# Kernel optimization log

Measured on AMD Instinct MI355X. Metric: run time of the kernel, lower is better.

Reference implementation:

```python
import jax, jax.numpy as jnp
import numpy as np
import math

D = 256
H = 128
GATE_IN = 2 * D + 1 + 1 + 3  # mu, logvar, s, minutes, snr(3) = 517


def setup_inputs() -> dict:
    key = jax.random.key(0)
    ks = jax.random.split(key, 10)
    B, S = 256, 512
    mu = jax.random.normal(ks[0], (B, S, D), dtype=jnp.float32)
    logvar = jax.random.normal(ks[1], (B, S, D), dtype=jnp.float32)
    minutes = jax.random.uniform(ks[2], (B, S), dtype=jnp.float32) * 120.0
    mu_c = jax.random.normal(ks[3], (2, D), dtype=jnp.float32) * 0.1
    log_tau2 = jax.random.normal(ks[4], (2, D), dtype=jnp.float32) * 0.1
    log_prior = jax.random.normal(ks[5], (2,), dtype=jnp.float32) * 0.1
    W1 = jax.random.normal(ks[6], (H, GATE_IN), dtype=jnp.float32) * 0.05
    b1 = jnp.zeros((H,), dtype=jnp.float32)
    W2 = jax.random.normal(ks[7], (1, H), dtype=jnp.float32) * 0.05
    b2 = jnp.zeros((1,), dtype=jnp.float32)
    alpha_logits = jnp.float32(0.0)          # logit(0.5)
    attn_lambda_logit = jnp.float32(0.0)     # logit(0.5)
    decay_rate_log = jnp.float32(math.log(0.1))
    return dict(mu=mu, logvar=logvar, minutes=minutes, mu_c=mu_c,
                log_tau2=log_tau2, log_prior=log_prior, W1=W1, b1=b1,
                W2=W2, b2=b2, alpha_logits=alpha_logits,
                attn_lambda_logit=attn_lambda_logit,
                decay_rate_log=decay_rate_log)


def _logit(p):
    return jnp.log(p) - jnp.log1p(-p)


def reference(mu, logvar, minutes, mu_c, log_tau2, log_prior,
              W1, b1, W2, b2, alpha_logits, attn_lambda_logit,
              decay_rate_log):
    var = jnp.exp(logvar)                              # [B,S,D]

    def ell(c):
        tau2 = jnp.exp(log_tau2[c])                    # [D]
        diff2 = (mu - mu_c[c]) ** 2
        return -0.5 * jnp.sum((var + diff2) / tau2 + log_tau2[c], axis=-1)

    s = (ell(1) + log_prior[1]) - (ell(0) + log_prior[0])   # [B,S]

    # SNR features
    var_c = jnp.clip(var, 1e-6, None)
    snr1 = jnp.linalg.norm(mu, axis=-1) / math.sqrt(mu.shape[-1])
    snr2 = jnp.mean(logvar, axis=-1)
    snr3 = jnp.mean(mu ** 2 / var_c, axis=-1)
    snr = jnp.stack([snr1, snr2, snr3], axis=-1)            # [B,S,3]

    gate_in = jnp.concatenate(
        [mu, logvar, s[..., None], minutes[..., None], snr], axis=-1)

    h = jax.nn.relu(jnp.einsum('bsf,hf->bsh', gate_in, W1) + b1)
    a_raw = jax.nn.sigmoid(jnp.einsum('bsh,oh->bso', h, W2) + b2)[..., 0]

    # precision attention mixture
    score = jnp.sum(mu ** 2 / var_c, axis=-1)               # [B,S]
    a_prec = jax.nn.softmax(score, axis=1)
    a_mlp = a_raw / jnp.clip(jnp.sum(a_raw, axis=1, keepdims=True), 1e-6, None)
    lam = jax.nn.sigmoid(attn_lambda_logit)
    a = lam * a_mlp + (1.0 - lam) * a_prec

    # time decay
    last_time = jnp.max(minutes, axis=1, keepdims=True)
    delta_h = jnp.clip(last_time - minutes, 0.0, None) / 60.0
    rate = jax.nn.softplus(decay_rate_log)
    w = a * jnp.exp(-rate * delta_h)
    a = w / jnp.clip(jnp.sum(w, axis=1, keepdims=True), 1e-6, None)

    # mean aggregator
    s_main = jnp.sum(a * s, axis=1)                         # [B]

    # Noisy-OR branch
    p_i = jnp.clip(jax.nn.sigmoid(s) * a, 1e-6, 1.0 - 1e-6)
    log1m = jnp.sum(jnp.log1p(-p_i), axis=1)
    p_or = 1.0 - jnp.exp(log1m)
    s_or = _logit(jnp.clip(p_or, 1e-6, 1.0 - 1e-6))

    alpha = jax.nn.sigmoid(alpha_logits)
    s_total = alpha * s_main + (1.0 - alpha) * s_or
    return (s_total, s, a)
```

## Files before the change

### kernel.cpp

```cpp
#include <hip/hip_runtime.h>
#include <hip/hip_bf16.h>

#define B_DIM 256
#define NTOK (256 * 512)
#define W1_LD 517
#define TPB 32

#define WS_DIT 0
#define WS_E 256
#define WS_C0 512
#define WS_W1F 1024
#define WS_W1X 17408
#define WS_SCORE 20480

typedef __attribute__((ext_vector_type(8))) short bf16x8;
typedef __attribute__((ext_vector_type(4))) float f32x4;
typedef long long i64;

__device__ __forceinline__ unsigned pk2(float a, float b) {
  __hip_bfloat162 h = __float22bfloat162_rn(make_float2(a, b));
  unsigned r;
  __builtin_memcpy(&r, &h, 4);
  return r;
}
__device__ __forceinline__ unsigned pk4f8(float a, float b, float c, float d) {
  int r = __builtin_amdgcn_cvt_pk_fp8_f32(a, b, 0, false);
  r = __builtin_amdgcn_cvt_pk_fp8_f32(c, d, r, true);
  return (unsigned)r;
}

template <int CTRL>
__device__ __forceinline__ float dpp_add(float v) {
  int s = __builtin_amdgcn_update_dpp(0, __float_as_int(v), CTRL, 0xf, 0xf,
                                      true);
  return v + __int_as_float(s);
}
__device__ __forceinline__ float row8_sum(float v) {
  v = dpp_add<0xB1>(v);
  v = dpp_add<0x4E>(v);
  v = dpp_add<0x141>(v);
  return v;
}
__device__ __forceinline__ float row16_sum(float v) {
  v = dpp_add<0xB1>(v);
  v = dpp_add<0x4E>(v);
  v = dpp_add<0x124>(v);
  v = dpp_add<0x128>(v);
  return v;
}

__device__ __forceinline__ float wave_sum(float v) {
#pragma unroll
  for (int off = 32; off > 0; off >>= 1) v += __shfl_xor(v, off, 64);
  return v;
}
__device__ __forceinline__ float wave_max(float v) {
#pragma unroll
  for (int off = 32; off > 0; off >>= 1) v = fmaxf(v, __shfl_xor(v, off, 64));
  return v;
}
__device__ __forceinline__ float block_sum(float v, float* scr) {
  v = wave_sum(v);
  int wid = threadIdx.x >> 6;
  __syncthreads();
  if ((threadIdx.x & 63) == 0) scr[wid] = v;
  __syncthreads();
  return scr[0] + scr[1] + scr[2] + scr[3];
}

__global__ __launch_bounds__(256) void k_setup(
    const float* __restrict__ W1, const float* __restrict__ b1,
    const float* __restrict__ mu_c, const float* __restrict__ log_tau2,
    const float* __restrict__ log_prior, float* __restrict__ wsc) {
  const int tid = threadIdx.x;
  const int h = blockIdx.x;
  const float* wr = W1 + h * W1_LD;
  {
    const int p = 2 * tid;
    const int c0 = ((p & 15) < 8) ? (p >> 4) * 8 + (p & 7)
                                  : 256 + (p >> 4) * 8 + (p & 7);
    const int p1 = p + 1;
    const int c1 = ((p1 & 15) < 8) ? (p1 >> 4) * 8 + (p1 & 7)
                                   : 256 + (p1 >> 4) * 8 + (p1 & 7);
    const int pk = __builtin_amdgcn_cvt_pk_fp8_f32(wr[c0], wr[c1], 0, false);
    char* w1f = (char*)(wsc + WS_W1F);
    const int off = (h >> 4) * 8192 + (p >> 5) * 512 +
                    (((p >> 3) & 3) * 16 + (h & 15)) * 8 + (p & 7);
    *(ushort*)(w1f + off) = (ushort)pk;
  }
  if (tid == 0) {
    ushort* w1x = (ushort*)(wsc + WS_W1X);
    const int nb = (h >> 4) * 512;
    uint4 g0;
    g0.x = pk2(wr[512], wr[513]);
    g0.y = pk2(wr[514], wr[515]);
    g0.z = pk2(wr[516], b1[h]);
    g0.w = 0u;
    *(uint4*)(w1x + nb + (h & 15) * 8) = g0;
    const uint4 z = {0u, 0u, 0u, 0u};
    *(uint4*)(w1x + nb + (16 + (h & 15)) * 8) = z;
    *(uint4*)(w1x + nb + (32 + (h & 15)) * 8) = z;
    *(uint4*)(w1x + nb + (48 + (h & 15)) * 8) = z;
  }

  if (blockIdx.x == 0) {
    __shared__ float scr[4];
    float lt0 = log_tau2[tid], lt1 = log_tau2[256 + tid];
    float mc0 = mu_c[tid], mc1 = mu_c[256 + tid];
    float it0 = __expf(-lt0), it1 = __expf(-lt1);
    wsc[WS_DIT + tid] = it1 - it0;
    wsc[WS_E + tid] = 2.0f * (mc1 * it1 - mc0 * it0);
    float g = mc1 * mc1 * it1 - mc0 * mc0 * it0 + (lt1 - lt0);
    float sg = block_sum(g, scr);
    if (tid == 0) wsc[WS_C0] = (log_prior[1] - log_prior[0]) - 0.5f * sg;
  }
}

__global__ __launch_bounds__(256, 8) void k_token(
    const float* __restrict__ mu, const float* __restrict__ logvar,
    const float* __restrict__ minutes, const float* __restrict__ W2g,
    const float* __restrict__ b2, const float* __restrict__ wsc,
    float* __restrict__ out_s, float* __restrict__ ws_score,
    float* __restrict__ araw_out) {
  __shared__ __align__(16) char A_l[TPB * 512];
  __shared__ __align__(16) ushort axl[TPB * 32];
  __shared__ float red2[4][TPB];

  const int tid = threadIdx.x;
  const int w = tid >> 6;
  const int l = tid & 63;
  const int tokbase = blockIdx.x * TPB;
  const float C0 = wsc[WS_C0];

  if (tid < 96) {
    const int row = tid & 31;
    const int c = tid >> 5;
    const uint4 z = {0u, 0u, 0u, 0u};
    *(uint4*)((char*)axl + row * 64 + 16 + c * 16) = z;
  }

  const int trow = tid >> 3;
  const int l8 = tid & 7;
  const int swz = (trow & 7) << 4;
  const size_t gbase = (size_t)(tokbase + trow) * 256 + l8 * 8;
  const float* ditg = wsc + WS_DIT + l8 * 8;
  const float* eg = wsc + WS_E + l8 * 8;
  float Ss = 0.f, Sm = 0.f, Sl = 0.f, Sc = 0.f;
#pragma unroll
  for (int t = 0; t < 4; ++t) {
    const float4 m0 = *(const float4*)(mu + gbase + t * 64);
    const float4 m1 = *(const float4*)(mu + gbase + t * 64 + 4);
    const float4 v0 = *(const float4*)(logvar + gbase + t * 64);
    const float4 v1 = *(const float4*)(logvar + gbase + t * 64 + 4);
    const float4 dA = *(const float4*)(ditg + t * 64);
    const float4 dB = *(const float4*)(ditg + t * 64 + 4);
    const float4 eA = *(const float4*)(eg + t * 64);
    const float4 eB = *(const float4*)(eg + t * 64 + 4);
#define CHUNK(m, lv, dt, ee)                                              \
  {                                                                       \
    const float va = __expf(lv.x), vb = __expf(lv.y), vc = __expf(lv.z),  \
                vd = __expf(lv.w);                                        \
    const float na = __expf(-lv.x), nb = __expf(-lv.y),                   \
                nc = __expf(-lv.z), nd = __expf(-lv.w);                   \
    const float qa = m.x * m.x, qb = m.y * m.y, qc = m.z * m.z,           \
                qd = m.w * m.w;                                           \
    Ss += (va + qa) * dt.x - m.x * ee.x + (vb + qb) * dt.y - m.y * ee.y + \
          (vc + qc) * dt.z - m.z * ee.z + (vd + qd) * dt.w - m.w * ee.w;  \
    Sm += qa + qb + qc + qd;                                              \
    Sl += lv.x + lv.y + lv.z + lv.w;                                      \
    Sc += qa * na + qb * nb + qc * nc + qd * nd;                          \
  }
    CHUNK(m0, v0, dA, eA);
    CHUNK(m1, v1, dB, eB);
#undef CHUNK
    uint4 u;
    u.x = pk4f8(m0.x, m0.y, m0.z, m0.w);
    u.y = pk4f8(m1.x, m1.y, m1.z, m1.w);
    u.z = pk4f8(v0.x, v0.y, v0.z, v0.w);
    u.w = pk4f8(v1.x, v1.y, v1.z, v1.w);
    const int col = trow * 512 + (t * 8 + l8) * 16;
    *(uint4*)(A_l + (col ^ swz)) = u;
  }
  Ss = row8_sum(Ss);
  Sm = row8_sum(Sm);
  Sl = row8_sum(Sl);
  Sc = row8_sum(Sc);
  if (l8 == 0) {
    const float sval = -0.5f * Ss + C0;
    const float mn = minutes[tokbase + trow];
    uint4 ex;
    ex.x = pk2(sval, mn);
    ex.y = pk2(sqrtf(Sm) * (1.0f / 16.0f), Sl * (1.0f / 256.0f));
    ex.z = pk2(Sc * (1.0f / 256.0f), 1.0f);
    ex.w = 0u;
    *(uint4*)((char*)axl + trow * 64) = ex;
    out_s[tokbase + trow] = sval;
    ws_score[tokbase + trow] = Sc;
  }
  __syncthreads();

  f32x4 a00 = {0.f, 0.f, 0.f, 0.f};
  f32x4 a01 = {0.f, 0.f, 0.f, 0.f};
  f32x4 a10 = {0.f, 0.f, 0.f, 0.f};
  f32x4 a11 = {0.f, 0.f, 0.f, 0.f};
  const int m_lane = l & 15;
  const int swzA = (m_lane & 7) << 4;
  const int rowA0 = m_lane * 512;
  const int rowA1 = rowA0 + 16 * 512;
  const char* w1f = (const char*)(wsc + WS_W1F);
  const char* bp0 = w1f + (2 * w) * 8192 + l * 8;
  const char* bp1 = bp0 + 8192;
#pragma unroll 4
  for (int ks = 0; ks < 16; ++ks) {
    const int kOff = ks * 32 + (l >> 4) * 8;
    i64 f0 = *(const i64*)(A_l + ((rowA0 + kOff) ^ swzA));
    i64 f1 = *(const i64*)(A_l + ((rowA1 + kOff) ^ swzA));
    i64 bq0 = *(const i64*)(bp0 + ks * 512);
    i64 bq1 = *(const i64*)(bp1 + ks * 512);
    a00 = __builtin_amdgcn_mfma_f32_16x16x32_fp8_fp8(f0, bq0, a00, 0, 0, 0);
    a01 = __builtin_amdgcn_mfma_f32_16x16x32_fp8_fp8(f0, bq1, a01, 0, 0, 0);
    a10 = __builtin_amdgcn_mfma_f32_16x16x32_fp8_fp8(f1, bq0, a10, 0, 0, 0);
    a11 = __builtin_amdgcn_mfma_f32_16x16x32_fp8_fp8(f1, bq1, a11, 0, 0, 0);
  }
  {
    const int xb = (l >> 4) * 16;
    bf16x8 f0 = *(const bf16x8*)((char*)axl + m_lane * 64 + xb);
    bf16x8 f1 = *(const bf16x8*)((char*)axl + (m_lane + 16) * 64 + xb);
    const ushort* w1x = (const ushort*)(wsc + WS_W1X);
    bf16x8 bq0 = *(const bf16x8*)(w1x + (2 * w) * 512 + l * 8);
    bf16x8 bq1 = *(const bf16x8*)(w1x + (2 * w + 1) * 512 + l * 8);
    a00 = __builtin_amdgcn_mfma_f32_16x16x32_bf16(f0, bq0, a00, 0, 0, 0);
    a01 = __builtin_amdgcn_mfma_f32_16x16x32_bf16(f0, bq1, a01, 0, 0, 0);
    a10 = __builtin_amdgcn_mfma_f32_16x16x32_bf16(f1, bq0, a10, 0, 0, 0);
    a11 = __builtin_amdgcn_mfma_f32_16x16x32_bf16(f1, bq1, a11, 0, 0, 0);
  }

  const int g = l >> 4;
  const float w2a = W2g[32 * w + m_lane];
  const float w2b = W2g[32 * w + m_lane + 16];
#pragma unroll
  for (int mf = 0; mf < 2; ++mf) {
    const f32x4 aN0 = mf ? a10 : a00;
    const f32x4 aN1 = mf ? a11 : a01;
#pragma unroll
    for (int r = 0; r < 4; ++r) {
      const int t_loc = 16 * mf + 4 * g + r;
      float cs = fmaxf(aN0[r], 0.f) * w2a + fmaxf(aN1[r], 0.f) * w2b;
      cs = row16_sum(cs);
      if (m_lane == 0) red2[w][t_loc] = cs;
    }
  }
  __syncthreads();
  if (tid < TPB) {
    float z = red2[0][tid] + red2[1][tid] + red2[2][tid] + red2[3][tid] +
              b2[0];
    araw_out[tokbase + tid] = 1.0f / (1.0f + __expf(-z));
  }
}

__global__ __launch_bounds__(256) void k_row(
    const float* __restrict__ minutes, const float* __restrict__ s_in,
    const float* __restrict__ score_in, float* a_io,
    const float* __restrict__ alpha_logits,
    const float* __restrict__ attn_lambda_logit,
    const float* __restrict__ decay_rate_log, float* __restrict__ out_total) {
  __shared__ float scrA[4][4];
  __shared__ float scrB[4];
  __shared__ float scrC[4];
  __shared__ float scrD[4][2];
  const int row = blockIdx.x;
  const int tid = threadIdx.x;
  const int w = tid >> 6;
  const int base = row * 512;
  const float sc0 = score_in[base + tid], sc1 = score_in[base + 256 + tid];
  const float sv0 = s_in[base + tid], sv1 = s_in[base + 256 + tid];
  const float ar0 = a_io[base + tid], ar1 = a_io[base + 256 + tid];
  const float mn0 = minutes[base + tid], mn1 = minutes[base + 256 + tid];

  const float vsc = wave_max(fmaxf(sc0, sc1));
  const float vmn = wave_max(fmaxf(mn0, mn1));
  const float var_ = wave_sum(ar0 + ar1);
  if ((tid & 63) == 0) {
    scrA[w][0] = vsc;
    scrA[w][1] = vmn;
    scrA[w][2] = var_;
  }
  __syncthreads();
  const float msc = fmaxf(fmaxf(scrA[0][0], scrA[1][0]),
                          fmaxf(scrA[2][0], scrA[3][0]));
  const float mmn = fmaxf(fmaxf(scrA[0][1], scrA[1][1]),
                          fmaxf(scrA[2][1], scrA[3][1]));
  const float sar = scrA[0][2] + scrA[1][2] + scrA[2][2] + scrA[3][2];

  const float e0 = __expf(sc0 - msc), e1 = __expf(sc1 - msc);
  const float vse = wave_sum(e0 + e1);
  if ((tid & 63) == 0) scrB[w] = vse;
  __syncthreads();
  const float se = scrB[0] + scrB[1] + scrB[2] + scrB[3];

  const float lam = 1.0f / (1.0f + __expf(-attn_lambda_logit[0]));
  const float alpha = 1.0f / (1.0f + __expf(-alpha_logits[0]));
  const float rate = log1pf(__expf(decay_rate_log[0]));

  const float inv_sar = 1.0f / fmaxf(sar, 1e-6f);
  const float inv_se = 1.0f / se;
  const float a00 = lam * ar0 * inv_sar + (1.0f - lam) * e0 * inv_se;
  const float a01 = lam * ar1 * inv_sar + (1.0f - lam) * e1 * inv_se;
  const float dh0 = fmaxf(mmn - mn0, 0.0f) * (1.0f / 60.0f);
  const float dh1 = fmaxf(mmn - mn1, 0.0f) * (1.0f / 60.0f);
  const float w0 = a00 * __expf(-rate * dh0);
  const float w1 = a01 * __expf(-rate * dh1);
  const float vsw = wave_sum(w0 + w1);
  if ((tid & 63) == 0) scrC[w] = vsw;
  __syncthreads();
  const float sw = scrC[0] + scrC[1] + scrC[2] + scrC[3];
  const float inv_sw = 1.0f / fmaxf(sw, 1e-6f);
  const float af0 = w0 * inv_sw, af1 = w1 * inv_sw;
  a_io[base + tid] = af0;
  a_io[base + 256 + tid] = af1;

  const float sg0 = 1.0f / (1.0f + __expf(-sv0));
  const float sg1 = 1.0f / (1.0f + __expf(-sv1));
  const float p0 = fminf(fmaxf(sg0 * af0, 1e-6f), 1.0f - 1e-6f);
  const float p1 = fminf(fmaxf(sg1 * af1, 1e-6f), 1.0f - 1e-6f);
  const float vsm = wave_sum(af0 * sv0 + af1 * sv1);
  const float vlg = wave_sum(log1pf(-p0) + log1pf(-p1));
  if ((tid & 63) == 0) {
    scrD[w][0] = vsm;
    scrD[w][1] = vlg;
  }
  __syncthreads();
  if (tid == 0) {
    const float smain = scrD[0][0] + scrD[1][0] + scrD[2][0] + scrD[3][0];
    const float slg = scrD[0][1] + scrD[1][1] + scrD[2][1] + scrD[3][1];
    float por = 1.0f - __expf(slg);
    por = fminf(fmaxf(por, 1e-6f), 1.0f - 1e-6f);
    const float sor = logf(por) - log1pf(-por);
    out_total[row] = alpha * smain + (1.0f - alpha) * sor;
  }
}

extern "C" void kernel_launch(void* const* d_in, const int* in_sizes, int n_in,
                              void* d_out, int out_size, void* d_ws,
                              size_t ws_size, hipStream_t stream) {
  const float* mu = (const float*)d_in[0];
  const float* logvar = (const float*)d_in[1];
  const float* minutes = (const float*)d_in[2];
  const float* mu_c = (const float*)d_in[3];
  const float* log_tau2 = (const float*)d_in[4];
  const float* log_prior = (const float*)d_in[5];
  const float* W1 = (const float*)d_in[6];
  const float* b1 = (const float*)d_in[7];
  const float* W2 = (const float*)d_in[8];
  const float* b2 = (const float*)d_in[9];
  const float* alpha_logits = (const float*)d_in[10];
  const float* attn_lambda_logit = (const float*)d_in[11];
  const float* decay_rate_log = (const float*)d_in[12];

  float* out = (float*)d_out;
  float* out_total = out;
  float* out_s = out + B_DIM;
  float* out_a = out + B_DIM + NTOK;
  float* wsc = (float*)d_ws;
  float* ws_score = wsc + WS_SCORE;

  k_setup<<<128, 256, 0, stream>>>(W1, b1, mu_c, log_tau2, log_prior, wsc);
  k_token<<<NTOK / TPB, 256, 0, stream>>>(mu, logvar, minutes, W2, b2, wsc,
                                          out_s, ws_score, out_a);
  k_row<<<B_DIM, 256, 0, stream>>>(minutes, out_s, ws_score, out_a,
                                   alpha_logits, attn_lambda_logit,
                                   decay_rate_log, out_total);
}
```

Baseline: 58.31 us.

## Double token tile to 64 with 8 waves each owning 16 hidden units

```diff
diff --git a/kernel.cpp b/kernel.cpp
--- a/kernel.cpp
+++ b/kernel.cpp
@@ -4,7 +4,7 @@
 #define B_DIM 256
 #define NTOK (256 * 512)
 #define W1_LD 517
-#define TPB 32
+#define TPB 64
 
 #define WS_DIT 0
 #define WS_E 256
@@ -116,7 +116,7 @@
   }
 }
 
-__global__ __launch_bounds__(256, 8) void k_token(
+__global__ __launch_bounds__(512, 8) void k_token(
     const float* __restrict__ mu, const float* __restrict__ logvar,
     const float* __restrict__ minutes, const float* __restrict__ W2g,
     const float* __restrict__ b2, const float* __restrict__ wsc,
@@ -124,7 +124,7 @@
     float* __restrict__ araw_out) {
   __shared__ __align__(16) char A_l[TPB * 512];
   __shared__ __align__(16) ushort axl[TPB * 32];
-  __shared__ float red2[4][TPB];
+  __shared__ float red2[8][TPB];
 
   const int tid = threadIdx.x;
   const int w = tid >> 6;
@@ -132,9 +132,9 @@
   const int tokbase = blockIdx.x * TPB;
   const float C0 = wsc[WS_C0];
 
-  if (tid < 96) {
-    const int row = tid & 31;
-    const int c = tid >> 5;
+  if (tid < 192) {
+    const int row = tid & 63;
+    const int c = tid >> 6;
     const uint4 z = {0u, 0u, 0u, 0u};
     *(uint4*)((char*)axl + row * 64 + 16 + c * 16) = z;
   }
@@ -199,53 +199,51 @@
   }
   __syncthreads();
 
-  f32x4 a00 = {0.f, 0.f, 0.f, 0.f};
-  f32x4 a01 = {0.f, 0.f, 0.f, 0.f};
-  f32x4 a10 = {0.f, 0.f, 0.f, 0.f};
-  f32x4 a11 = {0.f, 0.f, 0.f, 0.f};
+  f32x4 a0 = {0.f, 0.f, 0.f, 0.f};
+  f32x4 a1 = {0.f, 0.f, 0.f, 0.f};
+  f32x4 a2 = {0.f, 0.f, 0.f, 0.f};
+  f32x4 a3 = {0.f, 0.f, 0.f, 0.f};
   const int m_lane = l & 15;
   const int swzA = (m_lane & 7) << 4;
   const int rowA0 = m_lane * 512;
-  const int rowA1 = rowA0 + 16 * 512;
   const char* w1f = (const char*)(wsc + WS_W1F);
-  const char* bp0 = w1f + (2 * w) * 8192 + l * 8;
-  const char* bp1 = bp0 + 8192;
+  const char* bp = w1f + w * 8192 + l * 8;
 #pragma unroll 4
   for (int ks = 0; ks < 16; ++ks) {
     const int kOff = ks * 32 + (l >> 4) * 8;
+    i64 bq = *(const i64*)(bp + ks * 512);
     i64 f0 = *(const i64*)(A_l + ((rowA0 + kOff) ^ swzA));
-    i64 f1 = *(const i64*)(A_l + ((rowA1 + kOff) ^ swzA));
-    i64 bq0 = *(const i64*)(bp0 + ks * 512);
-    i64 bq1 = *(const i64*)(bp1 + ks * 512);
-    a00 = __builtin_amdgcn_mfma_f32_16x16x32_fp8_fp8(f0, bq0, a00, 0, 0, 0);
-    a01 = __builtin_amdgcn_mfma_f32_16x16x32_fp8_fp8(f0, bq1, a01, 0, 0, 0);
-    a10 = __builtin_amdgcn_mfma_f32_16x16x32_fp8_fp8(f1, bq0, a10, 0, 0, 0);
-    a11 = __builtin_amdgcn_mfma_f32_16x16x32_fp8_fp8(f1, bq1, a11, 0, 0, 0);
+    i64 f1 = *(const i64*)(A_l + ((rowA0 + 16 * 512 + kOff) ^ swzA));
+    i64 f2 = *(const i64*)(A_l + ((rowA0 + 32 * 512 + kOff) ^ swzA));
+    i64 f3 = *(const i64*)(A_l + ((rowA0 + 48 * 512 + kOff) ^ swzA));
+    a0 = __builtin_amdgcn_mfma_f32_16x16x32_fp8_fp8(f0, bq, a0, 0, 0, 0);
+    a1 = __builtin_amdgcn_mfma_f32_16x16x32_fp8_fp8(f1, bq, a1, 0, 0, 0);
+    a2 = __builtin_amdgcn_mfma_f32_16x16x32_fp8_fp8(f2, bq, a2, 0, 0, 0);
+    a3 = __builtin_amdgcn_mfma_f32_16x16x32_fp8_fp8(f3, bq, a3, 0, 0, 0);
   }
   {
     const int xb = (l >> 4) * 16;
+    const ushort* w1x = (const ushort*)(wsc + WS_W1X);
+    bf16x8 bq = *(const bf16x8*)(w1x + w * 512 + l * 8);
     bf16x8 f0 = *(const bf16x8*)((char*)axl + m_lane * 64 + xb);
     bf16x8 f1 = *(const bf16x8*)((char*)axl + (m_lane + 16) * 64 + xb);
-    const ushort* w1x = (const ushort*)(wsc + WS_W1X);
-    bf16x8 bq0 = *(const bf16x8*)(w1x + (2 * w) * 512 + l * 8);
-    bf16x8 bq1 = *(const bf16x8*)(w1x + (2 * w + 1) * 512 + l * 8);
-    a00 = __builtin_amdgcn_mfma_f32_16x16x32_bf16(f0, bq0, a00, 0, 0, 0);
-    a01 = __builtin_amdgcn_mfma_f32_16x16x32_bf16(f0, bq1, a01, 0, 0, 0);
-    a10 = __builtin_amdgcn_mfma_f32_16x16x32_bf16(f1, bq0, a10, 0, 0, 0);
-    a11 = __builtin_amdgcn_mfma_f32_16x16x32_bf16(f1, bq1, a11, 0, 0, 0);
+    bf16x8 f2 = *(const bf16x8*)((char*)axl + (m_lane + 32) * 64 + xb);
+    bf16x8 f3 = *(const bf16x8*)((char*)axl + (m_lane + 48) * 64 + xb);
+    a0 = __builtin_amdgcn_mfma_f32_16x16x32_bf16(f0, bq, a0, 0, 0, 0);
+    a1 = __builtin_amdgcn_mfma_f32_16x16x32_bf16(f1, bq, a1, 0, 0, 0);
+    a2 = __builtin_amdgcn_mfma_f32_16x16x32_bf16(f2, bq, a2, 0, 0, 0);
+    a3 = __builtin_amdgcn_mfma_f32_16x16x32_bf16(f3, bq, a3, 0, 0, 0);
   }
 
   const int g = l >> 4;
-  const float w2a = W2g[32 * w + m_lane];
-  const float w2b = W2g[32 * w + m_lane + 16];
-#pragma unroll
-  for (int mf = 0; mf < 2; ++mf) {
-    const f32x4 aN0 = mf ? a10 : a00;
-    const f32x4 aN1 = mf ? a11 : a01;
+  const float w2a = W2g[16 * w + m_lane];
+#pragma unroll
+  for (int mf = 0; mf < 4; ++mf) {
+    const f32x4 aN = (mf == 0) ? a0 : (mf == 1) ? a1 : (mf == 2) ? a2 : a3;
 #pragma unroll
     for (int r = 0; r < 4; ++r) {
       const int t_loc = 16 * mf + 4 * g + r;
-      float cs = fmaxf(aN0[r], 0.f) * w2a + fmaxf(aN1[r], 0.f) * w2b;
+      float cs = fmaxf(aN[r], 0.f) * w2a;
       cs = row16_sum(cs);
       if (m_lane == 0) red2[w][t_loc] = cs;
     }
@@ -253,6 +251,7 @@
   __syncthreads();
   if (tid < TPB) {
     float z = red2[0][tid] + red2[1][tid] + red2[2][tid] + red2[3][tid] +
+              red2[4][tid] + red2[5][tid] + red2[6][tid] + red2[7][tid] +
               b2[0];
     araw_out[tokbase + tid] = 1.0f / (1.0f + __expf(-z));
   }
@@ -365,7 +364,7 @@
   float* ws_score = wsc + WS_SCORE;
 
   k_setup<<<128, 256, 0, stream>>>(W1, b1, mu_c, log_tau2, log_prior, wsc);
-  k_token<<<NTOK / TPB, 256, 0, stream>>>(mu, logvar, minutes, W2, b2, wsc,
+  k_token<<<NTOK / TPB, 512, 0, stream>>>(mu, logvar, minutes, W2, b2, wsc,
                                           out_s, ws_score, out_a);
   k_row<<<B_DIM, 256, 0, stream>>>(minutes, out_s, ws_score, out_a,
                                    alpha_logits, attn_lambda_logit,
```

New measurement: 56.63 us (median of 2 runs). 2.9% less time.
